# Optimization experiments

Measured on AMD Instinct MI355X. Metric: run time of the kernel, lower is better.

The kernel has to match this reference:

```python
import jax, jax.numpy as jnp
import numpy as np

EMBED_DIM = 1024
B, S = 4, 2048


def setup_inputs() -> dict:
    key = jax.random.key(0)
    ks = jax.random.split(key, 7)
    scale = 1.0 / np.sqrt(EMBED_DIM)
    return {
        "x": jax.random.normal(ks[0], (B, S, EMBED_DIM), dtype=jnp.float32),
        "Wq": jax.random.normal(ks[1], (EMBED_DIM, EMBED_DIM), dtype=jnp.float32) * scale,
        "bq": jnp.zeros((EMBED_DIM,), dtype=jnp.float32),
        "Wk": jax.random.normal(ks[2], (EMBED_DIM, EMBED_DIM), dtype=jnp.float32) * scale,
        "bk": jnp.zeros((EMBED_DIM,), dtype=jnp.float32),
        "Wv": jax.random.normal(ks[3], (EMBED_DIM, EMBED_DIM), dtype=jnp.float32) * scale,
        "bv": jnp.zeros((EMBED_DIM,), dtype=jnp.float32),
    }


def reference(x, Wq, bq, Wk, bk, Wv, bv):
    d = x.shape[-1]
    # nn.Linear: x @ W.T + b (W stored as [out, in])
    q = jnp.einsum("bsd,ed->bse", x, Wq) + bq
    k = jnp.einsum("bsd,ed->bse", x, Wk) + bk
    v = jnp.einsum("bsd,ed->bse", x, Wv) + bv
    scores = jnp.einsum("bqd,bkd->bqk", q, k) / jnp.sqrt(jnp.float32(d))
    seq_len = x.shape[1]
    causal = jnp.tril(jnp.ones((seq_len, seq_len), dtype=bool))  # [S, S]
    scores = jnp.where(causal, scores, -jnp.inf)
    weights = jax.nn.softmax(scores, axis=-1)
    return jnp.einsum("bqk,bkd->bqd", weights, v)
```

## Files before the change

kernel.cpp:

```cpp
#include <hip/hip_runtime.h>


#define BM 128
#define BN 128
#define BK 64

typedef unsigned short u16;
typedef short  bf16x8 __attribute__((ext_vector_type(8)));
typedef unsigned short u16x8 __attribute__((ext_vector_type(8)));
typedef float  f32x4  __attribute__((ext_vector_type(4)));

__device__ __forceinline__ u16 f2bf(float f) {
  unsigned int u = __float_as_uint(f);
  u += 0x7FFFu + ((u >> 16) & 1u);
  return (u16)(u >> 16);
}

__device__ __forceinline__ void async_ld16(const void* g, void* l) {
  __builtin_amdgcn_global_load_lds(
      (__attribute__((address_space(1))) unsigned int*)g,
      (__attribute__((address_space(3))) unsigned int*)l, 16, 0, 0);
}

__device__ __forceinline__ void gemm_core(
    const u16* __restrict__ A, int lda,
    const u16* __restrict__ B, int ldb,
    int kLen, f32x4 (&acc)[4][4], u16* As, u16* Bs)
{
  const int tid = threadIdx.x;
  const int wave = tid >> 6;
  const int lane = tid & 63;
  const int lane16 = lane & 15;
  const int quad = lane >> 4;
  const int wm = wave >> 1, wn = wave & 1;

#pragma unroll
  for (int i = 0; i < 4; i++)
#pragma unroll
    for (int j = 0; j < 4; j++)
      acc[i][j] = (f32x4){0.f, 0.f, 0.f, 0.f};

  for (int k0 = 0; k0 < kLen; k0 += BK) {
    __syncthreads();
#pragma unroll
    for (int j = 0; j < 4; j++) {
      const int cbase = (wave * 4 + j) * 64;
      const int c = cbase + lane;
      const int row = c >> 3, kcp = c & 7;
      const int koff = k0 + ((kcp ^ (row & 7)) << 3);
      async_ld16(A + (size_t)row * lda + koff, As + cbase * 8);
      async_ld16(B + (size_t)row * ldb + koff, Bs + cbase * 8);
    }
    __syncthreads();

#pragma unroll
    for (int h = 0; h < 2; h++) {
      bf16x8 af[4], bfr[4];
#pragma unroll
      for (int i = 0; i < 4; i++) {
        const int ra = wm * 64 + i * 16 + lane16;
        const int rb = wn * 64 + i * 16 + lane16;
        const int kc = (h * 4 + quad);
        af[i]  = __builtin_bit_cast(bf16x8,
                   *(const u16x8*)(As + ra * BK + ((kc ^ (ra & 7)) << 3)));
        bfr[i] = __builtin_bit_cast(bf16x8,
                   *(const u16x8*)(Bs + rb * BK + ((kc ^ (rb & 7)) << 3)));
      }
#pragma unroll
      for (int i = 0; i < 4; i++)
#pragma unroll
        for (int j = 0; j < 4; j++)
          acc[i][j] = __builtin_amdgcn_mfma_f32_16x16x32_bf16(
              af[i], bfr[j], acc[i][j], 0, 0, 0);
    }
  }
}

__global__ void cast_all(const float* __restrict__ x,  const float* __restrict__ wq,
                         const float* __restrict__ wk, const float* __restrict__ wv,
                         u16* __restrict__ xb,  u16* __restrict__ wqb,
                         u16* __restrict__ wkb, u16* __restrict__ wvb,
                         float* __restrict__ rowsum) {
  const int b = blockIdx.x;
  if (b < 32) rowsum[b * 256 + threadIdx.x] = 0.f;
  const float* src; u16* dst; int i0;
  if (b < 8192)       { src = x;  dst = xb;  i0 = b; }
  else if (b < 9216)  { src = wq; dst = wqb; i0 = b - 8192; }
  else if (b < 10240) { src = wk; dst = wkb; i0 = b - 9216; }
  else                { src = wv; dst = wvb; i0 = b - 10240; }
  const int i = i0 * 256 + threadIdx.x;
  const float4 v = ((const float4*)src)[i];
  ushort4 o;
  o.x = f2bf(v.x); o.y = f2bf(v.y); o.z = f2bf(v.z); o.w = f2bf(v.w);
  ((ushort4*)dst)[i] = o;
}

__global__ void qkv_kernel(const u16* __restrict__ xb, const u16* __restrict__ Wqkb,
                           const u16* __restrict__ Wvb,
                           const float* __restrict__ bq, const float* __restrict__ bk,
                           const float* __restrict__ bv,
                           u16* __restrict__ Qb, u16* __restrict__ Kb,
                           u16* __restrict__ Vt) {
  __shared__ __align__(16) u16 As[BM * BK];
  __shared__ __align__(16) u16 Bs[BN * BK];
  const int bid = blockIdx.x;
  const int tid = threadIdx.x, wave = tid >> 6, lane = tid & 63;
  const int wm = wave >> 1, wn = wave & 1, lane16 = lane & 15, quad = lane >> 4;
  f32x4 acc[4][4];
  if (bid < 1024) {
    const int m0 = (bid >> 4) * BM, n0 = (bid & 15) * BN;
    gemm_core(xb + (size_t)m0 * 1024, 1024, Wqkb + (size_t)n0 * 1024, 1024, 1024,
              acc, As, Bs);
    const bool isQ = (n0 < 1024);
    const float scale = isQ ? 0.03125f : 1.0f;
    const float* bias = isQ ? bq : bk;
    u16* dst = isQ ? Qb : Kb;
    const int c0 = isQ ? n0 : n0 - 1024;
#pragma unroll
    for (int i = 0; i < 4; i++)
#pragma unroll
      for (int j = 0; j < 4; j++) {
        const int col = c0 + wn * 64 + j * 16 + lane16;
        const float bcol = bias[col];
#pragma unroll
        for (int r = 0; r < 4; r++) {
          const int row = m0 + wm * 64 + i * 16 + quad * 4 + r;
          dst[(size_t)row * 1024 + col] = f2bf((acc[i][j][r] + bcol) * scale);
        }
      }
  } else {
    const int b2 = bid - 1024;
    const int m0 = (b2 >> 6) * BM;
    const int n0 = (b2 & 63) * BN;
    gemm_core(Wvb + (size_t)m0 * 1024, 1024, xb + (size_t)n0 * 1024, 1024, 1024,
              acc, As, Bs);
#pragma unroll
    for (int i = 0; i < 4; i++)
#pragma unroll
      for (int r = 0; r < 4; r++) {
        const int e = m0 + wm * 64 + i * 16 + quad * 4 + r;
        const float be = bv[e];
#pragma unroll
        for (int j = 0; j < 4; j++) {
          const int col = n0 + wn * 64 + j * 16 + lane16;
          const int bb = col >> 11, s = col & 2047;
          Vt[((size_t)bb * 1024 + e) * 2048 + s] = f2bf(acc[i][j][r] + be);
        }
      }
  }
}

__global__ void scores_exp_kernel(const u16* __restrict__ Qb,
                                  const u16* __restrict__ Kb,
                                  u16* __restrict__ P, float* __restrict__ rowsum) {
  const int m0 = blockIdx.y * BM, n0 = blockIdx.x * BN;
  if (n0 > m0 + (BM - 1)) return;
  __shared__ __align__(16) u16 As[BM * BK];
  __shared__ __align__(16) u16 Bs[BN * BK];
  const int b = blockIdx.z;
  const u16* Q = Qb + (size_t)b * 2048 * 1024;
  const u16* K = Kb + (size_t)b * 2048 * 1024;
  u16* Pb = P + (size_t)b * 2048 * 2048;
  float* rs = rowsum + (size_t)b * 2048;
  f32x4 acc[4][4];
  gemm_core(Q + (size_t)m0 * 1024, 1024, K + (size_t)n0 * 1024, 1024, 1024,
            acc, As, Bs);
  const int tid = threadIdx.x, wave = tid >> 6, lane = tid & 63;
  const int wm = wave >> 1, wn = wave & 1, lane16 = lane & 15, quad = lane >> 4;
#pragma unroll
  for (int i = 0; i < 4; i++) {
#pragma unroll
    for (int r = 0; r < 4; r++) {
      const int row = m0 + wm * 64 + i * 16 + quad * 4 + r;
      float partial = 0.f;
#pragma unroll
      for (int j = 0; j < 4; j++) {
        const int col = n0 + wn * 64 + j * 16 + lane16;
        const float e = (col <= row) ? __expf(acc[i][j][r]) : 0.f;
        partial += e;
        Pb[(size_t)row * 2048 + col] = f2bf(e);
      }
#pragma unroll
      for (int off = 1; off < 16; off <<= 1)
        partial += __shfl_xor(partial, off, 64);
      if (lane16 == 0) atomicAdd(rs + row, partial);
    }
  }
}

__global__ void pv_kernel(const u16* __restrict__ P, const u16* __restrict__ Vt,
                          const float* __restrict__ rowsum,
                          float* __restrict__ out) {
  __shared__ __align__(16) u16 As[BM * BK];
  __shared__ __align__(16) u16 Bs[BN * BK];
  const int b = blockIdx.z;
  const int m0 = blockIdx.y * BM, n0 = blockIdx.x * BN;
  const int kLen = m0 + BM;
  const u16* Pb = P + (size_t)b * 2048 * 2048;
  const u16* Vb = Vt + (size_t)b * 1024 * 2048;
  const float* rs = rowsum + (size_t)b * 2048;
  f32x4 acc[4][4];
  gemm_core(Pb + (size_t)m0 * 2048, 2048, Vb + (size_t)n0 * 2048, 2048, kLen,
            acc, As, Bs);
  const int tid = threadIdx.x, wave = tid >> 6, lane = tid & 63;
  const int wm = wave >> 1, wn = wave & 1, lane16 = lane & 15, quad = lane >> 4;
  float* O = out + (size_t)b * 2048 * 1024;
#pragma unroll
  for (int i = 0; i < 4; i++)
#pragma unroll
    for (int r = 0; r < 4; r++) {
      const int row = m0 + wm * 64 + i * 16 + quad * 4 + r;
      const float inv = 1.0f / rs[row];
#pragma unroll
      for (int j = 0; j < 4; j++) {
        const int col = n0 + wn * 64 + j * 16 + lane16;
        O[(size_t)row * 1024 + col] = acc[i][j][r] * inv;
      }
    }
}

extern "C" void kernel_launch(void* const* d_in, const int* in_sizes, int n_in,
                              void* d_out, int out_size, void* d_ws, size_t ws_size,
                              hipStream_t stream) {
  const float* x  = (const float*)d_in[0];
  const float* Wq = (const float*)d_in[1];
  const float* bq = (const float*)d_in[2];
  const float* Wk = (const float*)d_in[3];
  const float* bk = (const float*)d_in[4];
  const float* Wv = (const float*)d_in[5];
  const float* bv = (const float*)d_in[6];
  float* out = (float*)d_out;

  char* ws = (char*)d_ws;
  const size_t SZ_QB = (size_t)8192 * 1024 * 2;
  const size_t SZ_P  = (size_t)4 * 2048 * 2048 * 2;
  u16* Qb = (u16*)(ws);
  u16* Kb = (u16*)(ws + SZ_QB);
  u16* Vt = (u16*)(ws + 2 * SZ_QB);
  u16* P  = (u16*)(ws + 3 * SZ_QB);
  u16* xb = (u16*)(ws + 3 * SZ_QB + SZ_P);
  u16* Wqb = xb + (size_t)8192 * 1024;
  u16* Wkb = Wqb + 1024 * 1024;
  u16* Wvb = Wkb + 1024 * 1024;
  float* rowsum = (float*)(Wvb + 1024 * 1024);

  cast_all<<<11264, 256, 0, stream>>>(x, Wq, Wk, Wv, xb, Wqb, Wkb, Wvb, rowsum);
  qkv_kernel<<<1536, 256, 0, stream>>>(xb, Wqb, Wvb, bq, bk, bv, Qb, Kb, Vt);
  scores_exp_kernel<<<dim3(16, 16, 4), 256, 0, stream>>>(Qb, Kb, P, rowsum);
  pv_kernel<<<dim3(8, 16, 4), 256, 0, stream>>>(P, Vt, rowsum, out);
}
```

Measured before the change: 226.8 us.

## Fuse scores and PV kernels into one launch with per-row-block completion flags

Merges the causal score/exp kernel and the P·V kernel into a single grid. Score blocks are enumerated over the lower triangle only, so no blocks launch just to exit, and each finished row block bumps an atomic counter. PV blocks spin on that counter before starting, so PV work overlaps with the tail of score computation and one launch boundary goes away. This relies on score blocks being scheduled before the waiting PV blocks (lower block ids) to avoid deadlock, and spinning blocks occupy CU slots while they wait.

```diff
diff --git a/kernel.cpp b/kernel.cpp
--- a/kernel.cpp
+++ b/kernel.cpp
@@ -80,9 +80,10 @@
                          const float* __restrict__ wk, const float* __restrict__ wv,
                          u16* __restrict__ xb,  u16* __restrict__ wqb,
                          u16* __restrict__ wkb, u16* __restrict__ wvb,
-                         float* __restrict__ rowsum) {
+                         float* __restrict__ rowsum, unsigned* __restrict__ flags) {
   const int b = blockIdx.x;
   if (b < 32) rowsum[b * 256 + threadIdx.x] = 0.f;
+  if (b == 32 && threadIdx.x < 64) flags[threadIdx.x] = 0u;
   const float* src; u16* dst; int i0;
   if (b < 8192)       { src = x;  dst = xb;  i0 = b; }
   else if (b < 9216)  { src = wq; dst = wqb; i0 = b - 8192; }
@@ -150,73 +151,85 @@
   }
 }
 
-__global__ void scores_exp_kernel(const u16* __restrict__ Qb,
-                                  const u16* __restrict__ Kb,
-                                  u16* __restrict__ P, float* __restrict__ rowsum) {
-  const int m0 = blockIdx.y * BM, n0 = blockIdx.x * BN;
-  if (n0 > m0 + (BM - 1)) return;
+__global__ void attn_kernel(const u16* __restrict__ Qb, const u16* __restrict__ Kb,
+                            u16* __restrict__ P, float* __restrict__ rowsum,
+                            unsigned* __restrict__ flags,
+                            const u16* __restrict__ Vt, float* __restrict__ out) {
   __shared__ __align__(16) u16 As[BM * BK];
   __shared__ __align__(16) u16 Bs[BN * BK];
-  const int b = blockIdx.z;
-  const u16* Q = Qb + (size_t)b * 2048 * 1024;
-  const u16* K = Kb + (size_t)b * 2048 * 1024;
-  u16* Pb = P + (size_t)b * 2048 * 2048;
-  float* rs = rowsum + (size_t)b * 2048;
-  f32x4 acc[4][4];
-  gemm_core(Q + (size_t)m0 * 1024, 1024, K + (size_t)n0 * 1024, 1024, 1024,
-            acc, As, Bs);
+  const int bid = blockIdx.x;
   const int tid = threadIdx.x, wave = tid >> 6, lane = tid & 63;
   const int wm = wave >> 1, wn = wave & 1, lane16 = lane & 15, quad = lane >> 4;
-#pragma unroll
-  for (int i = 0; i < 4; i++) {
-#pragma unroll
-    for (int r = 0; r < 4; r++) {
-      const int row = m0 + wm * 64 + i * 16 + quad * 4 + r;
-      float partial = 0.f;
-#pragma unroll
-      for (int j = 0; j < 4; j++) {
-        const int col = n0 + wn * 64 + j * 16 + lane16;
-        const float e = (col <= row) ? __expf(acc[i][j][r]) : 0.f;
-        partial += e;
-        Pb[(size_t)row * 2048 + col] = f2bf(e);
-      }
-#pragma unroll
-      for (int off = 1; off < 16; off <<= 1)
-        partial += __shfl_xor(partial, off, 64);
-      if (lane16 == 0) atomicAdd(rs + row, partial);
-    }
+  f32x4 acc[4][4];
+
+  if (bid < 544) {
+    const int b = bid & 3;
+    const int t = bid >> 2;
+    int r = (int)((sqrtf(8.f * t + 1.f) - 1.f) * 0.5f);
+    while ((r + 1) * (r + 2) / 2 <= t) r++;
+    while (r * (r + 1) / 2 > t) r--;
+    const int m0 = r * BM;
+    const int n0 = (t - r * (r + 1) / 2) * BN;
+    const u16* Q = Qb + (size_t)b * 2048 * 1024;
+    const u16* K = Kb + (size_t)b * 2048 * 1024;
+    u16* Pb = P + (size_t)b * 2048 * 2048;
+    float* rs = rowsum + (size_t)b * 2048;
+    gemm_core(Q + (size_t)m0 * 1024, 1024, K + (size_t)n0 * 1024, 1024, 1024,
+              acc, As, Bs);
+#pragma unroll
+    for (int i = 0; i < 4; i++) {
+#pragma unroll
+      for (int rr = 0; rr < 4; rr++) {
+        const int row = m0 + wm * 64 + i * 16 + quad * 4 + rr;
+        float partial = 0.f;
+#pragma unroll
+        for (int j = 0; j < 4; j++) {
+          const int col = n0 + wn * 64 + j * 16 + lane16;
+          const float e = (col <= row) ? __expf(acc[i][j][rr]) : 0.f;
+          partial += e;
+          Pb[(size_t)row * 2048 + col] = f2bf(e);
+        }
+#pragma unroll
+        for (int off = 1; off < 16; off <<= 1)
+          partial += __shfl_xor(partial, off, 64);
+        if (lane16 == 0) atomicAdd(rs + row, partial);
+      }
+    }
+    __threadfence();
+    __syncthreads();
+    if (tid == 0) atomicAdd(&flags[b * 16 + r], 1u);
+  } else {
+    const int bid2 = bid - 544;
+    const int b = bid2 & 3;
+    const int m = (bid2 >> 2) & 15;
+    const int n = bid2 >> 6;
+    const unsigned need = (unsigned)(m + 1);
+    if (tid == 0) {
+      while (atomicAdd(&flags[b * 16 + m], 0u) < need)
+        __builtin_amdgcn_s_sleep(2);
+    }
+    __syncthreads();
+    const int m0 = m * BM, n0 = n * BN;
+    const int kLen = m0 + BM;
+    const u16* Pb = P + (size_t)b * 2048 * 2048;
+    const u16* Vb = Vt + (size_t)b * 1024 * 2048;
+    const float* rs = rowsum + (size_t)b * 2048;
+    gemm_core(Pb + (size_t)m0 * 2048, 2048, Vb + (size_t)n0 * 2048, 2048, kLen,
+              acc, As, Bs);
+    float* O = out + (size_t)b * 2048 * 1024;
+#pragma unroll
+    for (int i = 0; i < 4; i++)
+#pragma unroll
+      for (int rr = 0; rr < 4; rr++) {
+        const int row = m0 + wm * 64 + i * 16 + quad * 4 + rr;
+        const float inv = 1.0f / rs[row];
+#pragma unroll
+        for (int j = 0; j < 4; j++) {
+          const int col = n0 + wn * 64 + j * 16 + lane16;
+          O[(size_t)row * 1024 + col] = acc[i][j][rr] * inv;
+        }
+      }
   }
-}
-
-__global__ void pv_kernel(const u16* __restrict__ P, const u16* __restrict__ Vt,
-                          const float* __restrict__ rowsum,
-                          float* __restrict__ out) {
-  __shared__ __align__(16) u16 As[BM * BK];
-  __shared__ __align__(16) u16 Bs[BN * BK];
-  const int b = blockIdx.z;
-  const int m0 = blockIdx.y * BM, n0 = blockIdx.x * BN;
-  const int kLen = m0 + BM;
-  const u16* Pb = P + (size_t)b * 2048 * 2048;
-  const u16* Vb = Vt + (size_t)b * 1024 * 2048;
-  const float* rs = rowsum + (size_t)b * 2048;
-  f32x4 acc[4][4];
-  gemm_core(Pb + (size_t)m0 * 2048, 2048, Vb + (size_t)n0 * 2048, 2048, kLen,
-            acc, As, Bs);
-  const int tid = threadIdx.x, wave = tid >> 6, lane = tid & 63;
-  const int wm = wave >> 1, wn = wave & 1, lane16 = lane & 15, quad = lane >> 4;
-  float* O = out + (size_t)b * 2048 * 1024;
-#pragma unroll
-  for (int i = 0; i < 4; i++)
-#pragma unroll
-    for (int r = 0; r < 4; r++) {
-      const int row = m0 + wm * 64 + i * 16 + quad * 4 + r;
-      const float inv = 1.0f / rs[row];
-#pragma unroll
-      for (int j = 0; j < 4; j++) {
-        const int col = n0 + wn * 64 + j * 16 + lane16;
-        O[(size_t)row * 1024 + col] = acc[i][j][r] * inv;
-      }
-    }
 }
 
 extern "C" void kernel_launch(void* const* d_in, const int* in_sizes, int n_in,
@@ -243,9 +256,10 @@
   u16* Wkb = Wqb + 1024 * 1024;
   u16* Wvb = Wkb + 1024 * 1024;
   float* rowsum = (float*)(Wvb + 1024 * 1024);
-
-  cast_all<<<11264, 256, 0, stream>>>(x, Wq, Wk, Wv, xb, Wqb, Wkb, Wvb, rowsum);
+  unsigned* flags = (unsigned*)(rowsum + 8192);
+
+  cast_all<<<11264, 256, 0, stream>>>(x, Wq, Wk, Wv, xb, Wqb, Wkb, Wvb,
+                                      rowsum, flags);
   qkv_kernel<<<1536, 256, 0, stream>>>(xb, Wqb, Wvb, bq, bk, bv, Qb, Kb, Vt);
-  scores_exp_kernel<<<dim3(16, 16, 4), 256, 0, stream>>>(Qb, Kb, P, rowsum);
-  pv_kernel<<<dim3(8, 16, 4), 256, 0, stream>>>(P, Vt, rowsum, out);
-}
+  attn_kernel<<<1056, 256, 0, stream>>>(Qb, Kb, P, rowsum, flags, Vt, out);
+}
```

Result: slower. 295.9 us (+30.4%).
